# Optimization experiments

Measured on AMD Instinct MI355X. Metric: run time of the kernel, lower is better.

The kernel has to match this reference:

```python
import jax, jax.numpy as jnp
import numpy as np

B, S, D = 4, 2048, 1024


def setup_inputs() -> dict:
    key = jax.random.key(0)
    ks = jax.random.split(key, 7)
    s = 1.0 / np.sqrt(D)
    return {
        "x": jax.random.normal(ks[0], (B, S, D), dtype=jnp.float32),
        "Wq": jax.random.normal(ks[1], (D, D), dtype=jnp.float32) * s,
        "bq": jnp.zeros((D,), dtype=jnp.float32),
        "Wk": jax.random.normal(ks[2], (D, D), dtype=jnp.float32) * s,
        "bk": jnp.zeros((D,), dtype=jnp.float32),
        "Wv": jax.random.normal(ks[3], (D, D), dtype=jnp.float32) * s,
        "bv": jnp.zeros((D,), dtype=jnp.float32),
    }


def reference(x, Wq, bq, Wk, bk, Wv, bv):
    # Linear layers: x @ W^T + b (torch nn.Linear convention)
    Q = jnp.einsum("bsd,ed->bse", x, Wq) + bq
    K = jnp.einsum("bsd,ed->bse", x, Wk) + bk
    V = jnp.einsum("bsd,ed->bse", x, Wv) + bv
    scale = 1.0 / (x.shape[-1] ** 0.5)
    scores = jnp.einsum("bse,bte->bst", Q, K) * scale  # [B, S, S]
    attn = jax.nn.softmax(scores, axis=-1)
    out = jnp.einsum("bst,bte->bse", attn, V)
    return out
```

## Files before the change

kernel.cpp:

```cpp
#include <hip/hip_runtime.h>
#include <math.h>


typedef _Float16 f16;
typedef _Float16 f16x8 __attribute__((ext_vector_type(8)));
typedef _Float16 f16x4 __attribute__((ext_vector_type(4)));
typedef float f32x4 __attribute__((ext_vector_type(4)));

__device__ __forceinline__ void glds16(const void* g, const void* l) {
    __builtin_amdgcn_global_load_lds(
        (const __attribute__((address_space(1))) void*)g,
        (__attribute__((address_space(3))) void*)l, 16, 0, 0);
}

#define VMCNT(n)  asm volatile("s_waitcnt vmcnt(" #n ")" ::: "memory")
#define LGKM(n)   asm volatile("s_waitcnt lgkmcnt(" #n ")" ::: "memory")
#define BARRIER() asm volatile("s_barrier" ::: "memory")
#define SCHEDB()  __builtin_amdgcn_sched_barrier(0)

__global__ __launch_bounds__(256) void prep_kernel(
    const float* __restrict__ x,
    const float* __restrict__ Wq, const float* __restrict__ Wk,
    const float* __restrict__ Wv,
    f16* __restrict__ xh, f16* __restrict__ Wh3, float* __restrict__ sums)
{
    const int bid = blockIdx.x, tid = threadIdx.x;
    if (bid < 8) {
        float4 z = {0.f, 0.f, 0.f, 0.f};
        ((float4*)sums)[bid * 256 + tid] = z;
    }
    if (bid < 8192) {
        const int i = bid * 256 + tid;
        float4 v = ((const float4*)x)[i];
        f16x4 h = { (f16)v.x, (f16)v.y, (f16)v.z, (f16)v.w };
        ((f16x4*)xh)[i] = h;
    } else {
        const int wid   = bid - 8192;
        const int plane = wid >> 10;
        const int i     = (wid & 1023) * 256 + tid;
        const float* src = (plane == 0) ? Wq : (plane == 1) ? Wk : Wv;
        float4 v = ((const float4*)src)[i];
        f16x4 h = { (f16)v.x, (f16)v.y, (f16)v.z, (f16)v.w };
        ((f16x4*)(Wh3 + (size_t)plane * 1024 * 1024))[i] = h;
    }
}

__global__ __launch_bounds__(512, 2) void qkv_fused_kernel(
    const f16* __restrict__ xh, const f16* __restrict__ Wh3,
    const float* __restrict__ bq, const float* __restrict__ bk,
    const float* __restrict__ bv,
    f16* __restrict__ Qh, f16* __restrict__ Kh, f16* __restrict__ Vt)
{
    extern __shared__ __align__(16) f16 smem[];
    const int bx = blockIdx.x >> 5;
    const int by = blockIdx.x & 31;
    const int m0 = by * 256;
    const int n0 = bx * 128;

    const int tid  = threadIdx.x;
    const int lane = tid & 63;
    const int w    = tid >> 6;
    const int wr   = w >> 1;
    const int wc   = w & 1;
    const int lr   = lane & 15;
    const int kq   = lane >> 4;

    const int rl = lane >> 3;
    const int ch = (lane & 7) ^ rl;

    unsigned oA[4];
    #pragma unroll
    for (int p = 0; p < 4; ++p)
        oA[p] = (unsigned)((m0 + p * 64 + w * 8 + rl) * 1024 + ch * 8);
    unsigned oB[6];
    #pragma unroll
    for (int p = 0; p < 6; ++p) {
        const int g  = w * 48 + p * 8;
        const int pl = g >> 7;
        const int rp = g & 127;
        oB[p] = (unsigned)(pl * 1048576 + (n0 + rp + rl) * 1024 + ch * 8);
    }

    f16* sA0 = smem;                f16* sA1 = smem + 16384;
    f16* sB0 = smem + 32768;        f16* sB1 = smem + 32768 + 24576;

    #define STAGEF(kofs, dA, dB) do {                                         \
        _Pragma("unroll")                                                     \
        for (int p = 0; p < 4; ++p)                                           \
            glds16(xh + oA[p] + (kofs), (dA) + w * 512 + p * 4096);           \
        _Pragma("unroll")                                                     \
        for (int p = 0; p < 6; ++p)                                           \
            glds16(Wh3 + oB[p] + (kofs), (dB) + w * 3072 + p * 512);          \
    } while (0)

    f32x4 aQ[4][4], aK[4][4], aV[4][4];
    #pragma unroll
    for (int i = 0; i < 4; ++i)
        #pragma unroll
        for (int j = 0; j < 4; ++j) {
            aQ[i][j] = (f32x4){0.f, 0.f, 0.f, 0.f};
            aK[i][j] = (f32x4){0.f, 0.f, 0.f, 0.f};
            aV[i][j] = (f32x4){0.f, 0.f, 0.f, 0.f};
        }

    STAGEF(0, sA0, sB0);
    f16* curA = sA0; f16* curB = sB0;
    f16* othA = sA1; f16* othB = sB1;

    for (int t = 0; t < 16; ++t) {
        if (t < 15) { STAGEF((t + 1) * 64, othA, othB); VMCNT(10); }
        else        { VMCNT(0); }
        BARRIER();

        #pragma unroll
        for (int kk = 0; kk < 2; ++kk) {
            const int c = kk * 4 + kq;
            f16x8 a[4];
            #pragma unroll
            for (int i = 0; i < 4; ++i) {
                const int ra = wr * 64 + i * 16 + lr;
                a[i] = *(const f16x8*)&curA[ra * 64 + ((c ^ (ra & 7)) * 8)];
            }
            #define ZBLOCK(zi, ACC, ISLAST) do {                              \
                f16x8 b[4];                                                   \
                _Pragma("unroll")                                             \
                for (int j = 0; j < 4; ++j) {                                 \
                    const int rb = (zi) * 128 + wc * 64 + j * 16 + lr;        \
                    b[j] = *(const f16x8*)&curB[rb * 64 + ((c ^ (rb & 7)) * 8)]; \
                }                                                             \
                LGKM(0);                                                      \
                if (ISLAST) BARRIER();          \
                SCHEDB();                                                     \
                __builtin_amdgcn_s_setprio(1);                                \
                _Pragma("unroll")                                             \
                for (int i = 0; i < 4; ++i)                                   \
                    _Pragma("unroll")                                         \
                    for (int j = 0; j < 4; ++j)                               \
                        ACC[i][j] = __builtin_amdgcn_mfma_f32_16x16x32_f16(   \
                            a[i], b[j], ACC[i][j], 0, 0, 0);                  \
                __builtin_amdgcn_s_setprio(0);                                \
            } while (0)

            ZBLOCK(0, aQ, false);
            ZBLOCK(1, aK, false);
            ZBLOCK(2, aV, kk == 1);
            #undef ZBLOCK
        }

        f16* xp;
        xp = curA; curA = othA; othA = xp;
        xp = curB; curB = othB; othB = xp;
    }
    #undef STAGEF

    const int col  = lr;
    const int quad = kq;
    #pragma unroll
    for (int j = 0; j < 4; ++j) {
        const int gn = n0 + wc * 64 + j * 16 + col;
        const float bbq = bq[gn];
        const float bbk = bk[gn];
        #pragma unroll
        for (int i = 0; i < 4; ++i)
            #pragma unroll
            for (int r = 0; r < 4; ++r) {
                const int gm = m0 + wr * 64 + i * 16 + quad * 4 + r;
                Qh[(size_t)gm * 1024 + gn] = (f16)((aQ[i][j][r] + bbq) * 0.03125f);
                Kh[(size_t)gm * 1024 + gn] = (f16)(aK[i][j][r] + bbk);
            }
    }
    #pragma unroll
    for (int i = 0; i < 4; ++i) {
        const int gmb = m0 + wr * 64 + i * 16 + quad * 4;
        const int bb_ = gmb >> 11;
        const int s   = gmb & 2047;
        f16* vtb = Vt + (size_t)bb_ * 1024 * 2048;
        #pragma unroll
        for (int j = 0; j < 4; ++j) {
            const int gn = n0 + wc * 64 + j * 16 + col;
            const float bbv = bv[gn];
            f16x4 v = { (f16)(aV[i][j][0] + bbv), (f16)(aV[i][j][1] + bbv),
                        (f16)(aV[i][j][2] + bbv), (f16)(aV[i][j][3] + bbv) };
            *(f16x4*)&vtb[(size_t)gn * 2048 + s] = v;
        }
    }
}

#define ABUF 16384
#define BBUF 8192
#define BOFF 49152

__device__ __forceinline__ void mfma_core3(
    const f16* A, int lda,
    const f16* B, int ldb,
    int K, int m0, int n0, f16* sm, f32x4 acc[4][4])
{
    const int tid  = threadIdx.x;
    const int lane = tid & 63;
    const int w    = tid >> 6;
    const int wr   = w >> 1;
    const int wc   = w & 1;
    const int lr   = lane & 15;
    const int kq   = lane >> 4;

    const int rl = lane >> 3;
    const int ch = (lane & 7) ^ rl;

    const f16* gA[4];
    #pragma unroll
    for (int p = 0; p < 4; ++p)
        gA[p] = A + (size_t)(m0 + p * 64 + w * 8 + rl) * lda + ch * 8;
    const f16* gB[2];
    #pragma unroll
    for (int p = 0; p < 2; ++p)
        gB[p] = B + (size_t)(n0 + p * 64 + w * 8 + rl) * ldb + ch * 8;

    const int NT = K >> 6;

    f16* sA0 = sm;             f16* sB0 = sm + BOFF;
    f16* sA1 = sm + ABUF;      f16* sB1 = sm + BOFF + BBUF;
    f16* sA2 = sm + 2 * ABUF;  f16* sB2 = sm + BOFF + 2 * BBUF;

    #define STAGE(kofs, dA, dB) do {                                          \
        _Pragma("unroll")                                                     \
        for (int p = 0; p < 4; ++p)                                           \
            glds16(gA[p] + (kofs), (dA) + w * 512 + p * 4096);                \
        _Pragma("unroll")                                                     \
        for (int p = 0; p < 2; ++p)                                           \
            glds16(gB[p] + (kofs), (dB) + w * 512 + p * 4096);                \
    } while (0)

    STAGE(0,  sA0, sB0);
    STAGE(64, sA1, sB1);

    int kst = 128;
    f16* curA = sA0; f16* curB = sB0;
    f16* nxtA = sA1; f16* nxtB = sB1;
    f16* farA = sA2; f16* farB = sB2;

    for (int t = 0; t < NT; ++t) {
        if (t + 2 < NT) {
            STAGE(kst, farA, farB);
            kst += 64;
            VMCNT(12);
        } else if (t + 1 < NT) {
            VMCNT(6);
        } else {
            VMCNT(0);
        }
        BARRIER();

        {
            f16x8 a[4], b[4];
            #pragma unroll
            for (int i = 0; i < 4; ++i) {
                const int ra = wr * 64 + i * 16 + lr;
                a[i] = *(const f16x8*)&curA[ra * 64 + ((kq ^ (ra & 7)) * 8)];
            }
            #pragma unroll
            for (int j = 0; j < 4; ++j) {
                const int rb = wc * 64 + j * 16 + lr;
                b[j] = *(const f16x8*)&curB[rb * 64 + ((kq ^ (rb & 7)) * 8)];
            }
            LGKM(0);
            SCHEDB();
            __builtin_amdgcn_s_setprio(1);
            #pragma unroll
            for (int i = 0; i < 4; ++i)
                #pragma unroll
                for (int j = 0; j < 4; ++j)
                    acc[i][j] = __builtin_amdgcn_mfma_f32_16x16x32_f16(a[i], b[j], acc[i][j], 0, 0, 0);
            __builtin_amdgcn_s_setprio(0);
        }
        {
            f16x8 a[4], b[4];
            const int c = 4 + kq;
            #pragma unroll
            for (int i = 0; i < 4; ++i) {
                const int ra = wr * 64 + i * 16 + lr;
                a[i] = *(const f16x8*)&curA[ra * 64 + ((c ^ (ra & 7)) * 8)];
            }
            #pragma unroll
            for (int j = 0; j < 4; ++j) {
                const int rb = wc * 64 + j * 16 + lr;
                b[j] = *(const f16x8*)&curB[rb * 64 + ((c ^ (rb & 7)) * 8)];
            }
            LGKM(0);
            BARRIER();
            SCHEDB();
            __builtin_amdgcn_s_setprio(1);
            #pragma unroll
            for (int i = 0; i < 4; ++i)
                #pragma unroll
                for (int j = 0; j < 4; ++j)
                    acc[i][j] = __builtin_amdgcn_mfma_f32_16x16x32_f16(a[i], b[j], acc[i][j], 0, 0, 0);
            __builtin_amdgcn_s_setprio(0);
        }

        f16* tA = curA; f16* tB = curB;
        curA = nxtA; curB = nxtB;
        nxtA = farA; nxtB = farB;
        farA = tA;   farB = tB;
    }
    #undef STAGE
}

__device__ __forceinline__ void mfma_core8w(
    const f16* A, int lda,
    const f16* B, int ldb,
    int K, int m0, int n0, f16* sm, f32x4 (&acc)[8][4])
{
    const int tid  = threadIdx.x;
    const int lane = tid & 63;
    const int w    = tid >> 6;
    const int wr   = w >> 2;
    const int wn   = w & 3;
    const int lr   = lane & 15;
    const int kq   = lane >> 4;

    const int rl = lane >> 3;
    const int ch = (lane & 7) ^ rl;

    const f16* gA[4];
    #pragma unroll
    for (int p = 0; p < 4; ++p)
        gA[p] = A + (size_t)(m0 + p * 64 + w * 8 + rl) * lda + ch * 8;
    const f16* gB[4];
    #pragma unroll
    for (int p = 0; p < 4; ++p)
        gB[p] = B + (size_t)(n0 + p * 64 + w * 8 + rl) * ldb + ch * 8;

    const int NT = K >> 6;

    f16* sA0 = sm;              f16* sA1 = sm + 16384;
    f16* sB0 = sm + 32768;      f16* sB1 = sm + 49152;

    #define STAGE8(kofs, dA, dB) do {                                         \
        _Pragma("unroll")                                                     \
        for (int p = 0; p < 4; ++p)                                           \
            glds16(gA[p] + (kofs), (dA) + w * 512 + p * 4096);                \
        _Pragma("unroll")                                                     \
        for (int p = 0; p < 4; ++p)                                           \
            glds16(gB[p] + (kofs), (dB) + w * 512 + p * 4096);                \
    } while (0)

    STAGE8(0, sA0, sB0);

    f16* curA = sA0; f16* curB = sB0;
    f16* othA = sA1; f16* othB = sB1;

    for (int t = 0; t < NT; ++t) {
        if (t + 1 < NT) {
            STAGE8((t + 1) * 64, othA, othB);
            VMCNT(8);
        } else {
            VMCNT(0);
        }
        BARRIER();

        #pragma unroll
        for (int kk = 0; kk < 2; ++kk) {
            f16x8 a[8], b[4];
            const int c = kk * 4 + kq;
            #pragma unroll
            for (int i = 0; i < 8; ++i) {
                const int ra = wr * 128 + i * 16 + lr;
                a[i] = *(const f16x8*)&curA[ra * 64 + ((c ^ (ra & 7)) * 8)];
            }
            #pragma unroll
            for (int j = 0; j < 4; ++j) {
                const int rb = wn * 64 + j * 16 + lr;
                b[j] = *(const f16x8*)&curB[rb * 64 + ((c ^ (rb & 7)) * 8)];
            }
            LGKM(0);
            if (kk == 1) BARRIER();
            SCHEDB();
            __builtin_amdgcn_s_setprio(1);
            #pragma unroll
            for (int i = 0; i < 8; ++i)
                #pragma unroll
                for (int j = 0; j < 4; ++j)
                    acc[i][j] = __builtin_amdgcn_mfma_f32_16x16x32_f16(a[i], b[j], acc[i][j], 0, 0, 0);
            __builtin_amdgcn_s_setprio(0);
        }

        f16* x;
        x = curA; curA = othA; othA = x;
        x = curB; curB = othB; othB = x;
    }
    #undef STAGE8
}

__global__ __launch_bounds__(512, 2) void scores_exp_kernel(
    const f16* __restrict__ Qh, const f16* __restrict__ Kh,
    f16* __restrict__ P, float* __restrict__ sums)
{
    extern __shared__ __align__(16) f16 smem[];
    const int b  = blockIdx.z;
    const int m0 = blockIdx.y * 256;
    const int n0 = blockIdx.x * 256;

    f32x4 acc[8][4];
    #pragma unroll
    for (int i = 0; i < 8; ++i)
        #pragma unroll
        for (int j = 0; j < 4; ++j) acc[i][j] = (f32x4){0.f, 0.f, 0.f, 0.f};

    const size_t ao = (size_t)b * 2048 * 1024;
    mfma_core8w(Qh + ao, 1024, Kh + ao, 1024, 1024, m0, n0, smem, acc);

    const int lane = threadIdx.x & 63;
    const int w    = threadIdx.x >> 6;
    const int wr = w >> 2, wn = w & 3;
    const int col  = lane & 15;
    const int quad = lane >> 4;
    f16* C = P + (size_t)b * 2048 * 2048;

    float rp[8][4];
    #pragma unroll
    for (int i = 0; i < 8; ++i)
        #pragma unroll
        for (int r = 0; r < 4; ++r) rp[i][r] = 0.0f;

    #pragma unroll
    for (int i = 0; i < 8; ++i)
        #pragma unroll
        for (int r = 0; r < 4; ++r) {
            const int gm = m0 + wr * 128 + i * 16 + quad * 4 + r;
            #pragma unroll
            for (int j = 0; j < 4; ++j) {
                const int gn = n0 + wn * 64 + j * 16 + col;
                const f16 p = (f16)__expf(acc[i][j][r]);
                C[(size_t)gm * 2048 + gn] = p;
                rp[i][r] += (float)p;
            }
        }

    #pragma unroll
    for (int i = 0; i < 8; ++i)
        #pragma unroll
        for (int r = 0; r < 4; ++r) {
            float v = rp[i][r];
            v += __shfl_xor(v, 1);
            v += __shfl_xor(v, 2);
            v += __shfl_xor(v, 4);
            v += __shfl_xor(v, 8);
            rp[i][r] = v;
        }
    if (col == 0) {
        #pragma unroll
        for (int i = 0; i < 8; ++i)
            #pragma unroll
            for (int r = 0; r < 4; ++r) {
                const int row = m0 + wr * 128 + i * 16 + quad * 4 + r;
                atomicAdd(&sums[b * 2048 + row], rp[i][r]);
            }
    }
}

__global__ __launch_bounds__(512) void pv_mfma_kernel(
    const f16* __restrict__ P, const f16* __restrict__ Vt,
    const float* __restrict__ sums, float* __restrict__ out)
{
    extern __shared__ __align__(16) f16 smem[];
    const int b  = blockIdx.z;
    const int m0 = blockIdx.y * 256;
    const int n0 = blockIdx.x * 128;

    f32x4 acc[4][4];
    #pragma unroll
    for (int i = 0; i < 4; ++i)
        #pragma unroll
        for (int j = 0; j < 4; ++j) acc[i][j] = (f32x4){0.f, 0.f, 0.f, 0.f};

    const size_t ao = (size_t)b * 2048 * 2048;
    const size_t bo = (size_t)b * 1024 * 2048;
    mfma_core3(P + ao, 2048, Vt + bo, 2048, 2048, m0, n0, smem, acc);

    const int lane = threadIdx.x & 63;
    const int w    = threadIdx.x >> 6;
    const int wm = (w >> 1) * 64;
    const int wn = (w & 1) * 64;
    const int col  = lane & 15;
    const int quad = lane >> 4;
    float* C = out + (size_t)b * 2048 * 1024;

    #pragma unroll
    for (int i = 0; i < 4; ++i)
        #pragma unroll
        for (int r = 0; r < 4; ++r) {
            const int rl = m0 + wm + i * 16 + quad * 4 + r;
            const float inv = 1.0f / sums[b * 2048 + rl];
            #pragma unroll
            for (int j = 0; j < 4; ++j) {
                const int gn = n0 + wn + j * 16 + col;
                C[(size_t)rl * 1024 + gn] = acc[i][j][r] * inv;
            }
        }
}

extern "C" void kernel_launch(void* const* d_in, const int* in_sizes, int n_in,
                              void* d_out, int out_size, void* d_ws, size_t ws_size,
                              hipStream_t stream)
{
    (void)in_sizes; (void)n_in; (void)out_size; (void)ws_size;
    const int Bn = 4, S = 2048, D = 1024;
    const float* x  = (const float*)d_in[0];
    const float* Wq = (const float*)d_in[1];
    const float* bq = (const float*)d_in[2];
    const float* Wk = (const float*)d_in[3];
    const float* bk = (const float*)d_in[4];
    const float* Wv = (const float*)d_in[5];
    const float* bv = (const float*)d_in[6];
    float* out = (float*)d_out;

    const size_t MB = 1024 * 1024;
    char* w = (char*)d_ws;
    f16*   xh   = (f16*)(w + 0 * MB);
    f16*   Wh3  = (f16*)(w + 16 * MB);
    f16*   Qh   = (f16*)(w + 38 * MB);
    f16*   Kh   = (f16*)(w + 54 * MB);
    f16*   Vt   = (f16*)(w + 70 * MB);
    float* sums = (float*)(w + 86 * MB);
    f16*   P    = (f16*)(w + 0 * MB);

    static bool attr_set = false;
    if (!attr_set) {
        (void)hipFuncSetAttribute(reinterpret_cast<const void*>(qkv_fused_kernel),
                            hipFuncAttributeMaxDynamicSharedMemorySize, 163840);
        (void)hipFuncSetAttribute(reinterpret_cast<const void*>(scores_exp_kernel),
                            hipFuncAttributeMaxDynamicSharedMemorySize, 131072);
        (void)hipFuncSetAttribute(reinterpret_cast<const void*>(pv_mfma_kernel),
                            hipFuncAttributeMaxDynamicSharedMemorySize, 147456);
        attr_set = true;
    }

    prep_kernel<<<dim3(11264), 256, 0, stream>>>(x, Wq, Wk, Wv, xh, Wh3, sums);

    qkv_fused_kernel<<<dim3(256), 512, 163840, stream>>>(
        xh, Wh3, bq, bk, bv, Qh, Kh, Vt);

    scores_exp_kernel<<<dim3(S / 256, S / 256, Bn), 512, 131072, stream>>>(
        Qh, Kh, P, sums);
    pv_mfma_kernel<<<dim3(D / 128, S / 256, Bn), 512, 147456, stream>>>(
        P, Vt, sums, out);
}
```

Baseline: 245.7 us.

## Split K across wave pairs in PV kernel and stagger LDS waits in QKV

The PV kernel now gives each pair of waves the two K-halves of one 64-wide stage, with each wave holding an 8x4 accumulator tile over 128 rows. The two halves are summed through LDS at the end, and the old shared mfma_core3 helper is inlined and removed. This is meant to raise MFMA work per LDS fragment load and cut the per-stage barrier count. The QKV projection loop also preloads the Q and K B-fragments and uses partial lgkmcnt waits so LDS reads overlap MFMAs. The costs are more registers (launch bounds 512,2) and an extra LDS reduction plus barrier.

```diff
diff --git a/kernel.cpp b/kernel.cpp
--- a/kernel.cpp
+++ b/kernel.cpp
@@ -115,36 +115,57 @@
         #pragma unroll
         for (int kk = 0; kk < 2; ++kk) {
             const int c = kk * 4 + kq;
-            f16x8 a[4];
+            f16x8 a[4], bQ[4], bK[4], bV[4];
             #pragma unroll
             for (int i = 0; i < 4; ++i) {
                 const int ra = wr * 64 + i * 16 + lr;
                 a[i] = *(const f16x8*)&curA[ra * 64 + ((c ^ (ra & 7)) * 8)];
             }
-            #define ZBLOCK(zi, ACC, ISLAST) do {                              \
-                f16x8 b[4];                                                   \
-                _Pragma("unroll")                                             \
-                for (int j = 0; j < 4; ++j) {                                 \
-                    const int rb = (zi) * 128 + wc * 64 + j * 16 + lr;        \
-                    b[j] = *(const f16x8*)&curB[rb * 64 + ((c ^ (rb & 7)) * 8)]; \
-                }                                                             \
-                LGKM(0);                                                      \
-                if (ISLAST) BARRIER();          \
-                SCHEDB();                                                     \
-                __builtin_amdgcn_s_setprio(1);                                \
-                _Pragma("unroll")                                             \
-                for (int i = 0; i < 4; ++i)                                   \
-                    _Pragma("unroll")                                         \
-                    for (int j = 0; j < 4; ++j)                               \
-                        ACC[i][j] = __builtin_amdgcn_mfma_f32_16x16x32_f16(   \
-                            a[i], b[j], ACC[i][j], 0, 0, 0);                  \
-                __builtin_amdgcn_s_setprio(0);                                \
-            } while (0)
-
-            ZBLOCK(0, aQ, false);
-            ZBLOCK(1, aK, false);
-            ZBLOCK(2, aV, kk == 1);
-            #undef ZBLOCK
+            #pragma unroll
+            for (int j = 0; j < 4; ++j) {
+                const int rb = wc * 64 + j * 16 + lr;
+                bQ[j] = *(const f16x8*)&curB[rb * 64 + ((c ^ (rb & 7)) * 8)];
+            }
+            #pragma unroll
+            for (int j = 0; j < 4; ++j) {
+                const int rb = 128 + wc * 64 + j * 16 + lr;
+                bK[j] = *(const f16x8*)&curB[rb * 64 + ((c ^ (rb & 7)) * 8)];
+            }
+            LGKM(4);
+            SCHEDB();
+            __builtin_amdgcn_s_setprio(1);
+            #pragma unroll
+            for (int i = 0; i < 4; ++i)
+                #pragma unroll
+                for (int j = 0; j < 4; ++j)
+                    aQ[i][j] = __builtin_amdgcn_mfma_f32_16x16x32_f16(a[i], bQ[j], aQ[i][j], 0, 0, 0);
+            __builtin_amdgcn_s_setprio(0);
+
+            #pragma unroll
+            for (int j = 0; j < 4; ++j) {
+                const int rb = 256 + wc * 64 + j * 16 + lr;
+                bV[j] = *(const f16x8*)&curB[rb * 64 + ((c ^ (rb & 7)) * 8)];
+            }
+            LGKM(4);
+            SCHEDB();
+            __builtin_amdgcn_s_setprio(1);
+            #pragma unroll
+            for (int i = 0; i < 4; ++i)
+                #pragma unroll
+                for (int j = 0; j < 4; ++j)
+                    aK[i][j] = __builtin_amdgcn_mfma_f32_16x16x32_f16(a[i], bK[j], aK[i][j], 0, 0, 0);
+            __builtin_amdgcn_s_setprio(0);
+
+            LGKM(0);
+            if (kk == 1) BARRIER();
+            SCHEDB();
+            __builtin_amdgcn_s_setprio(1);
+            #pragma unroll
+            for (int i = 0; i < 4; ++i)
+                #pragma unroll
+                for (int j = 0; j < 4; ++j)
+                    aV[i][j] = __builtin_amdgcn_mfma_f32_16x16x32_f16(a[i], bV[j], aV[i][j], 0, 0, 0);
+            __builtin_amdgcn_s_setprio(0);
         }
 
         f16* xp;
@@ -184,125 +205,6 @@
             *(f16x4*)&vtb[(size_t)gn * 2048 + s] = v;
         }
     }
-}
-
-#define ABUF 16384
-#define BBUF 8192
-#define BOFF 49152
-
-__device__ __forceinline__ void mfma_core3(
-    const f16* A, int lda,
-    const f16* B, int ldb,
-    int K, int m0, int n0, f16* sm, f32x4 acc[4][4])
-{
-    const int tid  = threadIdx.x;
-    const int lane = tid & 63;
-    const int w    = tid >> 6;
-    const int wr   = w >> 1;
-    const int wc   = w & 1;
-    const int lr   = lane & 15;
-    const int kq   = lane >> 4;
-
-    const int rl = lane >> 3;
-    const int ch = (lane & 7) ^ rl;
-
-    const f16* gA[4];
-    #pragma unroll
-    for (int p = 0; p < 4; ++p)
-        gA[p] = A + (size_t)(m0 + p * 64 + w * 8 + rl) * lda + ch * 8;
-    const f16* gB[2];
-    #pragma unroll
-    for (int p = 0; p < 2; ++p)
-        gB[p] = B + (size_t)(n0 + p * 64 + w * 8 + rl) * ldb + ch * 8;
-
-    const int NT = K >> 6;
-
-    f16* sA0 = sm;             f16* sB0 = sm + BOFF;
-    f16* sA1 = sm + ABUF;      f16* sB1 = sm + BOFF + BBUF;
-    f16* sA2 = sm + 2 * ABUF;  f16* sB2 = sm + BOFF + 2 * BBUF;
-
-    #define STAGE(kofs, dA, dB) do {                                          \
-        _Pragma("unroll")                                                     \
-        for (int p = 0; p < 4; ++p)                                           \
-            glds16(gA[p] + (kofs), (dA) + w * 512 + p * 4096);                \
-        _Pragma("unroll")                                                     \
-        for (int p = 0; p < 2; ++p)                                           \
-            glds16(gB[p] + (kofs), (dB) + w * 512 + p * 4096);                \
-    } while (0)
-
-    STAGE(0,  sA0, sB0);
-    STAGE(64, sA1, sB1);
-
-    int kst = 128;
-    f16* curA = sA0; f16* curB = sB0;
-    f16* nxtA = sA1; f16* nxtB = sB1;
-    f16* farA = sA2; f16* farB = sB2;
-
-    for (int t = 0; t < NT; ++t) {
-        if (t + 2 < NT) {
-            STAGE(kst, farA, farB);
-            kst += 64;
-            VMCNT(12);
-        } else if (t + 1 < NT) {
-            VMCNT(6);
-        } else {
-            VMCNT(0);
-        }
-        BARRIER();
-
-        {
-            f16x8 a[4], b[4];
-            #pragma unroll
-            for (int i = 0; i < 4; ++i) {
-                const int ra = wr * 64 + i * 16 + lr;
-                a[i] = *(const f16x8*)&curA[ra * 64 + ((kq ^ (ra & 7)) * 8)];
-            }
-            #pragma unroll
-            for (int j = 0; j < 4; ++j) {
-                const int rb = wc * 64 + j * 16 + lr;
-                b[j] = *(const f16x8*)&curB[rb * 64 + ((kq ^ (rb & 7)) * 8)];
-            }
-            LGKM(0);
-            SCHEDB();
-            __builtin_amdgcn_s_setprio(1);
-            #pragma unroll
-            for (int i = 0; i < 4; ++i)
-                #pragma unroll
-                for (int j = 0; j < 4; ++j)
-                    acc[i][j] = __builtin_amdgcn_mfma_f32_16x16x32_f16(a[i], b[j], acc[i][j], 0, 0, 0);
-            __builtin_amdgcn_s_setprio(0);
-        }
-        {
-            f16x8 a[4], b[4];
-            const int c = 4 + kq;
-            #pragma unroll
-            for (int i = 0; i < 4; ++i) {
-                const int ra = wr * 64 + i * 16 + lr;
-                a[i] = *(const f16x8*)&curA[ra * 64 + ((c ^ (ra & 7)) * 8)];
-            }
-            #pragma unroll
-            for (int j = 0; j < 4; ++j) {
-                const int rb = wc * 64 + j * 16 + lr;
-                b[j] = *(const f16x8*)&curB[rb * 64 + ((c ^ (rb & 7)) * 8)];
-            }
-            LGKM(0);
-            BARRIER();
-            SCHEDB();
-            __builtin_amdgcn_s_setprio(1);
-            #pragma unroll
-            for (int i = 0; i < 4; ++i)
-                #pragma unroll
-                for (int j = 0; j < 4; ++j)
-                    acc[i][j] = __builtin_amdgcn_mfma_f32_16x16x32_f16(a[i], b[j], acc[i][j], 0, 0, 0);
-            __builtin_amdgcn_s_setprio(0);
-        }
-
-        f16* tA = curA; f16* tB = curB;
-        curA = nxtA; curB = nxtB;
-        nxtA = farA; nxtB = farB;
-        farA = tA;   farB = tB;
-    }
-    #undef STAGE
 }
 
 __device__ __forceinline__ void mfma_core8w(
@@ -458,7 +360,11 @@
     }
 }
 
-__global__ __launch_bounds__(512) void pv_mfma_kernel(
+#define ABUF 16384
+#define BBUF 8192
+#define BOFF 49152
+
+__global__ __launch_bounds__(512, 2) void pv_mfma_kernel(
     const f16* __restrict__ P, const f16* __restrict__ Vt,
     const float* __restrict__ sums, float* __restrict__ out)
 {
@@ -467,36 +373,133 @@
     const int m0 = blockIdx.y * 256;
     const int n0 = blockIdx.x * 128;
 
-    f32x4 acc[4][4];
-    #pragma unroll
-    for (int i = 0; i < 4; ++i)
+    const int tid  = threadIdx.x;
+    const int lane = tid & 63;
+    const int w    = tid >> 6;
+    const int pos  = w >> 1;
+    const int ks   = w & 1;
+    const int wr2  = pos >> 1;
+    const int wc   = pos & 1;
+    const int lr   = lane & 15;
+    const int kq   = lane >> 4;
+    const int cb   = ks * 4 + kq;
+
+    const int rl = lane >> 3;
+    const int ch = (lane & 7) ^ rl;
+
+    const f16* A = P  + (size_t)b * 2048 * 2048;
+    const f16* B = Vt + (size_t)b * 1024 * 2048;
+
+    const f16* gA[4];
+    #pragma unroll
+    for (int p = 0; p < 4; ++p)
+        gA[p] = A + (size_t)(m0 + p * 64 + w * 8 + rl) * 2048 + ch * 8;
+    const f16* gB[2];
+    #pragma unroll
+    for (int p = 0; p < 2; ++p)
+        gB[p] = B + (size_t)(n0 + p * 64 + w * 8 + rl) * 2048 + ch * 8;
+
+    f16* sA0 = smem;             f16* sB0 = smem + BOFF;
+    f16* sA1 = smem + ABUF;      f16* sB1 = smem + BOFF + BBUF;
+    f16* sA2 = smem + 2 * ABUF;  f16* sB2 = smem + BOFF + 2 * BBUF;
+
+    #define STAGE(kofs, dA, dB) do {                                          \
+        _Pragma("unroll")                                                     \
+        for (int p = 0; p < 4; ++p)                                           \
+            glds16(gA[p] + (kofs), (dA) + w * 512 + p * 4096);                \
+        _Pragma("unroll")                                                     \
+        for (int p = 0; p < 2; ++p)                                           \
+            glds16(gB[p] + (kofs), (dB) + w * 512 + p * 4096);                \
+    } while (0)
+
+    f32x4 acc[8][4];
+    #pragma unroll
+    for (int i = 0; i < 8; ++i)
         #pragma unroll
         for (int j = 0; j < 4; ++j) acc[i][j] = (f32x4){0.f, 0.f, 0.f, 0.f};
 
-    const size_t ao = (size_t)b * 2048 * 2048;
-    const size_t bo = (size_t)b * 1024 * 2048;
-    mfma_core3(P + ao, 2048, Vt + bo, 2048, 2048, m0, n0, smem, acc);
-
-    const int lane = threadIdx.x & 63;
-    const int w    = threadIdx.x >> 6;
-    const int wm = (w >> 1) * 64;
-    const int wn = (w & 1) * 64;
-    const int col  = lane & 15;
-    const int quad = lane >> 4;
-    float* C = out + (size_t)b * 2048 * 1024;
-
-    #pragma unroll
-    for (int i = 0; i < 4; ++i)
-        #pragma unroll
-        for (int r = 0; r < 4; ++r) {
-            const int rl = m0 + wm + i * 16 + quad * 4 + r;
-            const float inv = 1.0f / sums[b * 2048 + rl];
+    STAGE(0,  sA0, sB0);
+    STAGE(64, sA1, sB1);
+
+    int kst = 128;
+    f16* curA = sA0; f16* curB = sB0;
+    f16* nxtA = sA1; f16* nxtB = sB1;
+    f16* farA = sA2; f16* farB = sB2;
+
+    const int NT = 32;
+    for (int t = 0; t < NT; ++t) {
+        if (t + 2 < NT) {
+            STAGE(kst, farA, farB);
+            kst += 64;
+            VMCNT(12);
+        } else if (t + 1 < NT) {
+            VMCNT(6);
+        } else {
+            VMCNT(0);
+        }
+        BARRIER();
+
+        f16x8 a[8], bb[4];
+        #pragma unroll
+        for (int i = 0; i < 8; ++i) {
+            const int ra = wr2 * 128 + i * 16 + lr;
+            a[i] = *(const f16x8*)&curA[ra * 64 + ((cb ^ (ra & 7)) * 8)];
+        }
+        #pragma unroll
+        for (int j = 0; j < 4; ++j) {
+            const int rb = wc * 64 + j * 16 + lr;
+            bb[j] = *(const f16x8*)&curB[rb * 64 + ((cb ^ (rb & 7)) * 8)];
+        }
+        LGKM(0);
+        BARRIER();
+        SCHEDB();
+        __builtin_amdgcn_s_setprio(1);
+        #pragma unroll
+        for (int i = 0; i < 8; ++i)
+            #pragma unroll
+            for (int j = 0; j < 4; ++j)
+                acc[i][j] = __builtin_amdgcn_mfma_f32_16x16x32_f16(a[i], bb[j], acc[i][j], 0, 0, 0);
+        __builtin_amdgcn_s_setprio(0);
+
+        f16* tA = curA; f16* tB = curB;
+        curA = nxtA; curB = nxtB;
+        nxtA = farA; nxtB = farB;
+        farA = tA;   farB = tB;
+    }
+    #undef STAGE
+
+    float* red = (float*)smem;
+    if (ks == 1) {
+        #pragma unroll
+        for (int i = 0; i < 8; ++i)
+            #pragma unroll
+            for (int j = 0; j < 4; ++j)
+                *(f32x4*)&red[(size_t)pos * 8192 + ((i * 4 + j) * 64 + lane) * 4] = acc[i][j];
+        LGKM(0);
+    }
+    BARRIER();
+
+    if (ks == 0) {
+        float* C = out + (size_t)b * 2048 * 1024;
+        #pragma unroll
+        for (int i = 0; i < 8; ++i) {
             #pragma unroll
             for (int j = 0; j < 4; ++j) {
-                const int gn = n0 + wn + j * 16 + col;
-                C[(size_t)rl * 1024 + gn] = acc[i][j][r] * inv;
-            }
-        }
+                f32x4 r4 = *(const f32x4*)&red[(size_t)pos * 8192 + ((i * 4 + j) * 64 + lane) * 4];
+                acc[i][j] += r4;
+            }
+            #pragma unroll
+            for (int r = 0; r < 4; ++r) {
+                const int grow = m0 + wr2 * 128 + i * 16 + kq * 4 + r;
+                const float inv = 1.0f / sums[b * 2048 + grow];
+                #pragma unroll
+                for (int j = 0; j < 4; ++j) {
+                    const int gn = n0 + wc * 64 + j * 16 + lr;
+                    C[(size_t)grow * 1024 + gn] = acc[i][j][r] * inv;
+                }
+            }
+        }
+    }
 }
 
 extern "C" void kernel_launch(void* const* d_in, const int* in_sizes, int n_in,
```

After: 275.9 us. 1.12x slower.
